# Performance work log

Measured on AMD Instinct MI355X. Metric: run time of the kernel, lower is better.

Reference implementation:

```python
import jax, jax.numpy as jnp
import numpy as np
import math

B, C, T = 4, 512, 2048
LN_EPS = 1e-5

def setup_inputs() -> dict:
    key = jax.random.key(0)
    ks = jax.random.split(key, 12)
    s = 1.0 / math.sqrt(C)
    inp = {
        'feat': jax.random.normal(ks[0], (B, C, T), dtype=jnp.float32),
        'Wq': jax.random.normal(ks[1], (C, C), dtype=jnp.float32) * s,
        'bq': jax.random.normal(ks[2], (C,), dtype=jnp.float32) * s,
        'Wk': jax.random.normal(ks[3], (C, C), dtype=jnp.float32) * s,
        'bk': jax.random.normal(ks[4], (C,), dtype=jnp.float32) * s,
        'Wv': jax.random.normal(ks[5], (C, C), dtype=jnp.float32) * s,
        'bv': jax.random.normal(ks[6], (C,), dtype=jnp.float32) * s,
        'Ws': jax.random.normal(ks[7], (C, C), dtype=jnp.float32) * s,
        'bs': jax.random.normal(ks[8], (C,), dtype=jnp.float32) * s,
        'Wl': jax.random.normal(ks[9], (C,), dtype=jnp.float32) * s,
        'bl': jax.random.normal(ks[10], (1,), dtype=jnp.float32) * s,
    }
    return inp

def reference(feat, Wq, bq, Wk, bk, Wv, bv, Ws, bs, Wl, bl):
    d = feat.shape[1]
    # 1x1 Conv1d == per-position linear over channels. feat: [B,C,T]
    value = jnp.einsum('oc,bct->bto', Wv, feat) + bv          # [B,T,C]
    query = jnp.einsum('oc,bct->bto', Wq, feat) + bq          # [B,T,C]
    key_  = jnp.einsum('oc,bct->bct', Wk, feat) + bk[:, None] # [B,C,T]
    f = jnp.einsum('btc,bcs->bts', query, key_) / math.sqrt(d)
    f = jax.nn.softmax(f, axis=2)                             # [B,T,T]
    y = jnp.einsum('bts,bsc->btc', f, value)                  # [B,T,C]
    f_score = jax.nn.sigmoid(jnp.einsum('btc,c->bt', y, Wl) + bl[0])
    z = jnp.einsum('bts,bsc->btc', 1.0 - f, value)            # [B,T,C]
    b_score = 1.0 - jax.nn.sigmoid(jnp.einsum('btc,c->bt', z, Wl) + bl[0])
    f_score = (f_score + b_score) / 2.0
    y_ct = jnp.einsum('oc,btc->bot', Ws, y) + bs[:, None]     # smooth conv, [B,C,T]
    out = feat + y_ct
    # LayerNorm over (C, T) jointly, default affine (weight=1, bias=0)
    mu = jnp.mean(out, axis=(1, 2), keepdims=True)
    var = jnp.mean(jnp.square(out - mu), axis=(1, 2), keepdims=True)
    out = (out - mu) * jax.lax.rsqrt(var + LN_EPS)
    return out, f_score
```

## Files before the change

### kernel.cpp

```cpp
#include <hip/hip_runtime.h>
#include <hip/hip_bf16.h>

#define BB 4
#define CC 512
#define TT 2048
static constexpr long CT  = (long)CC * TT;
static constexpr long TC  = (long)TT * CC;
static constexpr long TTT = (long)TT * TT;
static constexpr float SM_SCALE = 0.04419417382415922f;

typedef __bf16 bf16;
typedef __attribute__((ext_vector_type(8))) __bf16 bf16x8;
typedef __attribute__((ext_vector_type(4))) __bf16 bf16x4;
typedef __attribute__((ext_vector_type(4))) float f32x4;

__device__ __forceinline__ void load_lds16(const bf16* g, bf16* l)
{
    __builtin_amdgcn_global_load_lds(
        (const __attribute__((address_space(1))) void*)g,
        (__attribute__((address_space(3))) void*)l, 16, 0, 0);
}

template <int TM, int TN, int WR, int WC, int BK>
struct Core {
    static constexpr int THREADS = WR * WC * 64;
    static constexpr int MI = TM / (WR * 16);
    static constexpr int NI = TN / (WC * 16);
    static constexpr int CPR = BK / 8;
    static constexpr int RSH = (BK == 64) ? 3 : 2;
    static constexpr int CMASK = CPR - 1;
    static constexpr int CHUNKS = (TM + TN) * CPR;
    static constexpr int ACH = TM * CPR;
    static constexpr int CPT = CHUNKS / THREADS;
    static_assert(CPT * THREADS == CHUNKS, "chunk divisibility");

    __device__ static __forceinline__ void run(
        const bf16* __restrict__ Ab, const bf16* __restrict__ Bb,
        int K, int m0, int n0, bf16* As, bf16* Bs, f32x4 (&acc)[MI][NI])
    {
        const int tid  = threadIdx.x;
        const int lane = tid & 63;
        const int wid  = tid >> 6;
        const int wr = (wid / WC) * (MI * 16);
        const int wc = (wid % WC) * (NI * 16);
        const int lm = lane & 15;
        const int lq = lane >> 4;
        for (int k0 = 0; k0 < K; k0 += BK) {
#pragma unroll
            for (int i = 0; i < CPT; ++i) {
                int c = tid + i * THREADS;
                if (c < ACH) {
                    int row = c >> RSH;
                    int gc  = (c & CMASK) ^ (row & CMASK);
                    load_lds16(Ab + (long)(m0 + row) * K + k0 + gc * 8, As + c * 8);
                } else {
                    int d = c - ACH;
                    int row = d >> RSH;
                    int gc  = (d & CMASK) ^ (row & CMASK);
                    load_lds16(Bb + (long)(n0 + row) * K + k0 + gc * 8, Bs + d * 8);
                }
            }
            __syncthreads();
#pragma unroll
            for (int ks = 0; ks < BK / 32; ++ks) {
                bf16x8 af[MI], bfr[NI];
#pragma unroll
                for (int i = 0; i < MI; ++i) {
                    int ar = wr + i * 16 + lm;
                    int cc = (ks * 4 + lq) ^ (ar & CMASK);
                    af[i] = *(const bf16x8*)(As + ar * BK + cc * 8);
                }
#pragma unroll
                for (int i = 0; i < NI; ++i) {
                    int br = wc + i * 16 + lm;
                    int cc = (ks * 4 + lq) ^ (br & CMASK);
                    bfr[i] = *(const bf16x8*)(Bs + br * BK + cc * 8);
                }
#pragma unroll
                for (int mi = 0; mi < MI; ++mi)
#pragma unroll
                    for (int ni = 0; ni < NI; ++ni)
                        acc[mi][ni] = __builtin_amdgcn_mfma_f32_16x16x32_bf16(
                            af[mi], bfr[ni], acc[mi][ni], 0, 0, 0);
            }
            __syncthreads();
        }
    }
};

using CO = Core<128, 128, 4, 2, 64>;

struct CoreQV {
    static constexpr int THREADS = 512;
    static constexpr int MI = 2;
    static constexpr int NI = 4;
    static constexpr int BK = 64;
    static constexpr int CPR = 8, RSH = 3, CMASK = 7;
    static constexpr int ACH = 128 * 8;
    static constexpr int CHUNKS = 256 * 8;
    static constexpr int CPT = CHUNKS / THREADS;

    __device__ static __forceinline__ void run(
        const bf16* __restrict__ Ab, const bf16* __restrict__ Bq,
        const bf16* __restrict__ Bv,
        int m0, bf16* As, bf16* Bs, f32x4 (&acc)[MI][NI])
    {
        const int tid  = threadIdx.x;
        const int lane = tid & 63;
        const int wid  = tid >> 6;
        const int wr = (wid / 2) * 32;
        const int wc = (wid % 2) * 64;
        const int lm = lane & 15;
        const int lq = lane >> 4;
        for (int k0 = 0; k0 < 512; k0 += BK) {
#pragma unroll
            for (int i = 0; i < CPT; ++i) {
                int c = tid + i * THREADS;
                if (c < ACH) {
                    int row = c >> RSH;
                    int gc  = (c & CMASK) ^ (row & CMASK);
                    load_lds16(Ab + (long)(m0 + row) * 512 + k0 + gc * 8, As + c * 8);
                } else {
                    int d = c - ACH;
                    int row = d >> RSH;
                    int gc  = (d & CMASK) ^ (row & CMASK);
                    const bf16* src = (row < 64)
                        ? Bq + (long)row * 512
                        : Bv + (long)(row - 64) * 512;
                    load_lds16(src + k0 + gc * 8, Bs + d * 8);
                }
            }
            __syncthreads();
#pragma unroll
            for (int ks = 0; ks < 2; ++ks) {
                bf16x8 af[MI], bfr[NI];
#pragma unroll
                for (int i = 0; i < MI; ++i) {
                    int ar = wr + i * 16 + lm;
                    int cc = (ks * 4 + lq) ^ (ar & CMASK);
                    af[i] = *(const bf16x8*)(As + ar * BK + cc * 8);
                }
#pragma unroll
                for (int i = 0; i < NI; ++i) {
                    int br = wc + i * 16 + lm;
                    int cc = (ks * 4 + lq) ^ (br & CMASK);
                    bfr[i] = *(const bf16x8*)(Bs + br * BK + cc * 8);
                }
#pragma unroll
                for (int mi = 0; mi < MI; ++mi)
#pragma unroll
                    for (int ni = 0; ni < NI; ++ni)
                        acc[mi][ni] = __builtin_amdgcn_mfma_f32_16x16x32_bf16(
                            af[mi], bfr[ni], acc[mi][ni], 0, 0, 0);
            }
            __syncthreads();
        }
    }
};

__global__ __launch_bounds__(512)
void gemm_qv_kernel(const bf16* __restrict__ featT, const bf16* __restrict__ Wq_bf,
                    const bf16* __restrict__ Wv_bf, bf16* __restrict__ Qb,
                    bf16* __restrict__ Vn, const float* __restrict__ bq,
                    const float* __restrict__ bv, const float* __restrict__ wkc,
                    const float* __restrict__ bk, float* __restrict__ qb,
                    const float* __restrict__ Wl, float* __restrict__ vl)
{
    __shared__ bf16 As[128 * 64];
    __shared__ bf16 Bs[128 * 64];
    const int rb = blockIdx.z;
    const int m0 = blockIdx.y * 128;
    const int ng = blockIdx.x;
    const long wofs = (long)(ng * 64) * 512;
    f32x4 acc[2][4] = {};
    CoreQV::run(featT + (long)rb * TC, Wq_bf + wofs, Wv_bf + wofs, m0, As, Bs, acc);

    const int lane = threadIdx.x & 63, wid = threadIdx.x >> 6;
    const int wr = (wid / 2) * 32;
    const bool isV = wid & 1;
    const int lm = lane & 15, lq = lane >> 4;

    if (isV) {
        bf16* outV = Vn + (long)rb * TC;
        float* vlb = vl + (long)rb * TT;
        float vs_[2][4] = {};
#pragma unroll
        for (int mi = 0; mi < 2; ++mi)
#pragma unroll
            for (int ni = 0; ni < 4; ++ni) {
                int n = ng * 64 + ni * 16 + lm;
                float bn = bv[n], wn = Wl[n];
#pragma unroll
                for (int r = 0; r < 4; ++r) {
                    int m = m0 + wr + mi * 16 + lq * 4 + r;
                    float v = acc[mi][ni][r] + bn;
                    outV[(long)m * 512 + n] = (bf16)v;
                    vs_[mi][r] += v * wn;
                }
            }
#pragma unroll
        for (int mi = 0; mi < 2; ++mi)
#pragma unroll
            for (int r = 0; r < 4; ++r) {
                float s = vs_[mi][r];
                s += __shfl_xor(s, 1, 64); s += __shfl_xor(s, 2, 64);
                s += __shfl_xor(s, 4, 64); s += __shfl_xor(s, 8, 64);
                if (lm == 0)
                    atomicAdd(vlb + m0 + wr + mi * 16 + lq * 4 + r, s);
            }
    } else {
        bf16* out = Qb + (long)rb * TC;
        float* qbb = qb + (long)rb * TT;
        float rs[2][4] = {};
#pragma unroll
        for (int mi = 0; mi < 2; ++mi)
#pragma unroll
            for (int ni = 0; ni < 4; ++ni) {
                int n = ng * 64 + ni * 16 + lm;
                float bn = bq[n], wn = wkc[n], kn = bk[n];
#pragma unroll
                for (int r = 0; r < 4; ++r) {
                    int m = m0 + wr + mi * 16 + lq * 4 + r;
                    float v = acc[mi][ni][r] + bn;
                    rs[mi][r] += v * kn;
                    out[(long)m * 512 + n] = (bf16)(v * wn);
                }
            }
#pragma unroll
        for (int mi = 0; mi < 2; ++mi)
#pragma unroll
            for (int r = 0; r < 4; ++r) {
                float s = rs[mi][r];
                s += __shfl_xor(s, 1, 64); s += __shfl_xor(s, 2, 64);
                s += __shfl_xor(s, 4, 64); s += __shfl_xor(s, 8, 64);
                if (lm == 0)
                    atomicAdd(qbb + m0 + wr + mi * 16 + lq * 4 + r, s);
            }
    }
}

__global__ __launch_bounds__(512, 2)
void gemm_s256_kernel(const bf16* __restrict__ Qb, const bf16* __restrict__ featT,
                      bf16* __restrict__ S, const float* __restrict__ qb,
                      float* __restrict__ rsum, const float* __restrict__ vl,
                      float* __restrict__ u)
{
    __shared__ __align__(16) bf16 lds[2][2][256 * 64];
    const int id   = blockIdx.x;
    const int xcd  = id & 7, sIdx = id >> 3;
    const int bz   = xcd >> 1;
    const int n0   = (sIdx & 7) * 256;
    const int m0   = (((xcd & 1) << 2) + (sIdx >> 3)) * 256;
    const bf16* __restrict__ Ab = Qb + (long)bz * TC;
    const bf16* __restrict__ Bb = featT + (long)bz * TC;

    const int tid  = threadIdx.x;
    const int lane = tid & 63;
    const int wid  = tid >> 6;
    const int lm = lane & 15, lq = lane >> 4;
    const int wrb = (wid >> 2) * 64;
    const int wcb = (wid & 3) * 32;

    f32x4 acc[8][4] = {};

#define FENCE asm volatile("" ::: "memory")

#define STAGE_HT(t, op, h)                                                    \
    do {                                                                      \
        const bf16* gp_ = (op) ? Bb : Ab;                                     \
        const int  br_  = ((op) ? n0 : m0) + (h) * 128;                       \
        bf16* lp_ = &lds[(t) & 1][op][(h) * 128 * 64];                        \
        _Pragma("unroll")                                                     \
        for (int i_ = 0; i_ < 2; ++i_) {                                      \
            int c_ = tid + i_ * 512;                                          \
            int r_ = c_ >> 3;                                                 \
            int g_ = (c_ & 7) ^ (r_ & 7);                                     \
            load_lds16(gp_ + (long)(br_ + r_) * 512 + (t) * 64 + g_ * 8,      \
                       lp_ + c_ * 8);                                         \
        }                                                                     \
    } while (0)

#define PHASE(t, qm, qn, doSt, st, sop, sh, doVm)                             \
    do {                                                                      \
        bf16x8 af[2][4], bfr[2][2];                                           \
        const bf16* Al_ = lds[(t) & 1][0];                                    \
        const bf16* Bl_ = lds[(t) & 1][1];                                    \
        _Pragma("unroll")                                                     \
        for (int ks = 0; ks < 2; ++ks) {                                      \
            _Pragma("unroll")                                                 \
            for (int j = 0; j < 4; ++j) {                                     \
                int ar = (qm) * 128 + wrb + j * 16 + lm;                      \
                int cc = (ks * 4 + lq) ^ (ar & 7);                            \
                af[ks][j] = *(const bf16x8*)(Al_ + ar * 64 + cc * 8);         \
            }                                                                 \
            _Pragma("unroll")                                                 \
            for (int j = 0; j < 2; ++j) {                                     \
                int br = (qn) * 128 + wcb + j * 16 + lm;                      \
                int cc = (ks * 4 + lq) ^ (br & 7);                            \
                bfr[ks][j] = *(const bf16x8*)(Bl_ + br * 64 + cc * 8);        \
            }                                                                 \
        }                                                                     \
        if (doSt) STAGE_HT(st, sop, sh);                                      \
        if (doVm) {                                                           \
            if ((t) < 6) asm volatile("s_waitcnt vmcnt(4)" ::: "memory");     \
            else         asm volatile("s_waitcnt vmcnt(0)" ::: "memory");     \
        }                                                                     \
        FENCE; __builtin_amdgcn_s_barrier(); FENCE;                           \
        __builtin_amdgcn_s_setprio(1);                                        \
        _Pragma("unroll")                                                     \
        for (int ks = 0; ks < 2; ++ks)                                        \
            _Pragma("unroll")                                                 \
            for (int j = 0; j < 4; ++j)                                       \
                _Pragma("unroll")                                             \
                for (int j2 = 0; j2 < 2; ++j2)                                \
                    acc[(qm) * 4 + j][(qn) * 2 + j2] =                        \
                        __builtin_amdgcn_mfma_f32_16x16x32_bf16(              \
                            af[ks][j], bfr[ks][j2],                           \
                            acc[(qm) * 4 + j][(qn) * 2 + j2], 0, 0, 0);       \
        __builtin_amdgcn_s_setprio(0);                                        \
        FENCE; __builtin_amdgcn_s_barrier(); FENCE;                           \
    } while (0)

    STAGE_HT(0, 0, 0); STAGE_HT(0, 1, 0); STAGE_HT(0, 0, 1); STAGE_HT(0, 1, 1);
    STAGE_HT(1, 0, 0); STAGE_HT(1, 1, 0);
    asm volatile("s_waitcnt vmcnt(4)" ::: "memory");
    FENCE; __builtin_amdgcn_s_barrier(); FENCE;

    for (int t = 0; t < 8; ++t) {
        PHASE(t, 0, 0, t + 1 < 8, t + 1, 0, 1, false);
        PHASE(t, 0, 1, t + 1 < 8, t + 1, 1, 1, false);
        PHASE(t, 1, 0, t + 2 < 8, t + 2, 0, 0, false);
        PHASE(t, 1, 1, t + 2 < 8, t + 2, 1, 0, true);
    }
#undef PHASE
#undef STAGE_HT
#undef FENCE

    bf16* outp = S + (long)bz * TTT;
    const float* qbb = qb + (long)bz * TT;
    const float* vlb = vl + (long)bz * TT;
    float* rsb = rsum + (long)bz * TT;
    float* ub  = u + (long)bz * TT;
#pragma unroll
    for (int mi = 0; mi < 8; ++mi) {
        const int mrow = m0 + (mi >> 2) * 128 + wrb + (mi & 3) * 16 + lq * 4;
        const f32x4 qv = *(const f32x4*)(qbb + mrow);
        float rp[4] = {0.f, 0.f, 0.f, 0.f};
        float up[4] = {0.f, 0.f, 0.f, 0.f};
#pragma unroll
        for (int ni = 0; ni < 4; ++ni) {
            const int ncol = n0 + (ni >> 1) * 128 + wcb + (ni & 1) * 16 + lm;
            const float vlv = vlb[ncol];
#pragma unroll
            for (int r = 0; r < 4; ++r) {
                float p = __expf((acc[mi][ni][r] + qv[r]) * SM_SCALE);
                outp[(long)(mrow + r) * 2048 + ncol] = (bf16)p;
                rp[r] += p;
                up[r] += p * vlv;
            }
        }
#pragma unroll
        for (int r = 0; r < 4; ++r) {
            float s2 = rp[r], s3 = up[r];
            s2 += __shfl_xor(s2, 1, 64); s2 += __shfl_xor(s2, 2, 64);
            s2 += __shfl_xor(s2, 4, 64); s2 += __shfl_xor(s2, 8, 64);
            s3 += __shfl_xor(s3, 1, 64); s3 += __shfl_xor(s3, 2, 64);
            s3 += __shfl_xor(s3, 4, 64); s3 += __shfl_xor(s3, 8, 64);
            if (lm == 0) {
                atomicAdd(rsb + mrow + r, s2);
                atomicAdd(ub + mrow + r, s3);
            }
        }
    }
}

__global__ __launch_bounds__(512)
void gemm_vs_kernel(const bf16* __restrict__ Vn, const bf16* __restrict__ Ws_bf,
                    bf16* __restrict__ Vpt)
{
    __shared__ bf16 As[128 * 64];
    __shared__ bf16 Bs[128 * 64];
    const int id = blockIdx.x;
    const int xcd = id & 7, s = id >> 3;
    const int bz = xcd >> 1;
    const int m0 = (((xcd & 1) << 1) + (s >> 4)) * 128;
    const int n0 = (s & 15) * 128;
    f32x4 acc[2][4] = {};
    CO::run(Ws_bf, Vn + (long)bz * TC, 512, m0, n0, As, Bs, acc);

    const int lane = threadIdx.x & 63, wid = threadIdx.x >> 6;
    const int wr = (wid / 2) * 32, wc = (wid % 2) * 64;
    const int lm = lane & 15, lq = lane >> 4;
    bf16* out = Vpt + (long)bz * CT;
#pragma unroll
    for (int mi = 0; mi < 2; ++mi)
#pragma unroll
        for (int ni = 0; ni < 4; ++ni) {
            int n = n0 + wc + ni * 16 + lm;
#pragma unroll
            for (int r = 0; r < 4; ++r) {
                int m = m0 + wr + mi * 16 + lq * 4 + r;
                out[(long)m * 2048 + n] = (bf16)acc[mi][ni][r];
            }
        }
}

__global__ __launch_bounds__(512)
void gemm_out_kernel(const bf16* __restrict__ S, const bf16* __restrict__ Vpt,
                     float* __restrict__ out, const float* __restrict__ bs,
                     const float* __restrict__ feat,
                     const float* __restrict__ rsum, double* __restrict__ stats)
{
    __shared__ bf16 As[128 * 64];
    __shared__ bf16 Bs[128 * 64];
    __shared__ float red[16];
    const int id = blockIdx.x;
    const int xcd = id & 7, s = id >> 3;
    const int bz = xcd >> 1;
    const int n0 = (s & 3) * 128;
    const int m0 = (((xcd & 1) << 3) + (s >> 2)) * 128;
    f32x4 acc[2][4] = {};
    CO::run(S + (long)bz * TTT, Vpt + (long)bz * CT, 2048, m0, n0, As, Bs, acc);

    const int tid = threadIdx.x;
    const int lane = tid & 63, wid = tid >> 6;
    const int wr = (wid / 2) * 32, wc = (wid % 2) * 64;
    const int lm = lane & 15, lq = lane >> 4;
    const float* rsb = rsum + (long)bz * TT;
    float inv[2][4];
#pragma unroll
    for (int mi = 0; mi < 2; ++mi) {
        int mrow = m0 + wr + mi * 16 + lq * 4;
        f32x4 rv = *(const f32x4*)(rsb + mrow);
#pragma unroll
        for (int r = 0; r < 4; ++r) inv[mi][r] = 1.f / rv[r];
    }
    float s1 = 0.f, s2 = 0.f;
#pragma unroll
    for (int mi = 0; mi < 2; ++mi)
#pragma unroll
        for (int ni = 0; ni < 4; ++ni) {
            int mrow = m0 + wr + mi * 16 + lq * 4;
            int n = n0 + wc + ni * 16 + lm;
            long off = (long)bz * CT + (long)n * TT + mrow;
            f32x4 fv = *(const f32x4*)(feat + off);
            float bn = bs[n];
            f32x4 res;
#pragma unroll
            for (int r = 0; r < 4; ++r) {
                float v = acc[mi][ni][r] * inv[mi][r] + bn + fv[r];
                res[r] = v;
                s1 += v;
                s2 += v * v;
            }
            *(f32x4*)(out + off) = res;
        }
#pragma unroll
    for (int off = 32; off; off >>= 1) {
        s1 += __shfl_xor(s1, off, 64);
        s2 += __shfl_xor(s2, off, 64);
    }
    if (lane == 0) { red[wid] = s1; red[8 + wid] = s2; }
    __syncthreads();
    if (tid == 0) {
        double t1 = 0.0, t2 = 0.0;
#pragma unroll
        for (int w = 0; w < 8; ++w) { t1 += red[w]; t2 += red[8 + w]; }
        atomicAdd(stats + bz * 2, t1);
        atomicAdd(stats + bz * 2 + 1, t2);
    }
}

__global__ __launch_bounds__(256)
void prep_kernel(const float* __restrict__ feat, bf16* __restrict__ featT,
                 const float* __restrict__ Wq, const float* __restrict__ Wv,
                 const float* __restrict__ Ws, bf16* __restrict__ Wbf,
                 const float* __restrict__ Wk, const float* __restrict__ Wl,
                 const float* __restrict__ bv, float* __restrict__ wkc,
                 float* __restrict__ wvl, float* __restrict__ wlbv,
                 float* __restrict__ frp, float* __restrict__ qb,
                 float* __restrict__ u, float* __restrict__ rsum,
                 double* __restrict__ stats, float* __restrict__ vl)
{
    const int blk = blockIdx.x;
    const int tid = threadIdx.x;
    if (blk < 4096) {
        __shared__ float tile[32][33];
        __shared__ float sfr[4][32];
        const int b  = blk >> 10;
        const int c0 = ((blk & 1023) >> 6) * 32;
        const int tt = blk & 63;
        const int t0 = tt * 32;
        const int tx = tid & 31;
        const int ty = tid >> 5;
#pragma unroll
        for (int j = 0; j < 4; ++j) {
            int c = c0 + ty + j * 8;
            tile[ty + j * 8][tx] = feat[(long)b * CT + (long)c * TT + t0 + tx];
        }
        __syncthreads();
        float ps = 0.f;
#pragma unroll
        for (int j = 0; j < 4; ++j) {
            int tl = ty + j * 8;
            int t = t0 + tl;
            int c = c0 + tx;
            float v = tile[tx][tl];
            ps += v;
            featT[(long)b * TC + (long)t * CC + c] = (bf16)v;
        }
        const int wid = tid >> 6;
        ps += __shfl_xor(ps, 32, 64);
        if ((tid & 63) < 32) sfr[wid][tx] = ps;
        __syncthreads();
        if (tid < 32) {
            float s = sfr[0][tid] + sfr[1][tid] + sfr[2][tid] + sfr[3][tid];
            frp[(((long)b * 64 + tt) << 9) + c0 + tid] = s;
        }
    } else if (blk < 4480) {
        long gid = (long)(blk - 4096) * 256 + tid;
        long idx = gid * 8;
        int w = (int)(idx >> 18);
        long off = idx & 262143;
        const float* src = (w == 0) ? Wq : (w == 1) ? Wv : Ws;
        f32x4 a = *(const f32x4*)(src + off);
        f32x4 b = *(const f32x4*)(src + off + 4);
        bf16x8 o;
#pragma unroll
        for (int j = 0; j < 4; ++j) { o[j] = (bf16)a[j]; o[4 + j] = (bf16)b[j]; }
        *(bf16x8*)(Wbf + idx) = o;
    } else {
        int mid = (blk - 4480) * 256 + tid;
        if (mid < 512) {
            float s = 0.f;
            for (int o = 0; o < 512; ++o) s += Wk[o * 512 + mid];
            wkc[mid] = s;
        } else if (mid < 1024) {
            int k = mid - 512;
            float s = 0.f;
            for (int c = 0; c < 512; ++c) s += Wl[c] * Wv[c * 512 + k];
            wvl[k] = s;
        } else if (mid < 1088) {
            int lane = mid - 1024;
            float s = 0.f;
#pragma unroll
            for (int j = 0; j < 8; ++j) s += Wl[lane + 64 * j] * bv[lane + 64 * j];
#pragma unroll
            for (int off = 32; off; off >>= 1) s += __shfl_xor(s, off, 64);
            if (lane == 0) wlbv[0] = s;
        } else if (mid >= 1152 && mid < 1160) {
            stats[mid - 1152] = 0.0;
        } else if (mid >= 4096 && mid < 12288) {
            qb[mid - 4096] = 0.f;
        } else if (mid >= 12288 && mid < 20480) {
            u[mid - 12288] = 0.f;
        } else if (mid >= 20480 && mid < 28672) {
            rsum[mid - 20480] = 0.f;
        } else if (mid >= 28672 && mid < 36864) {
            vl[mid - 28672] = 0.f;
        }
    }
}

__global__ __launch_bounds__(256)
void ln_score_kernel(float* __restrict__ out, const double* __restrict__ stats,
                     const float* __restrict__ u, const float* __restrict__ frp,
                     const float* __restrict__ wvl, const float* __restrict__ wlbv,
                     const float* __restrict__ blp, const float* __restrict__ rsum)
{
    if (blockIdx.x < 4096) {
        long i = ((long)blockIdx.x * 256 + threadIdx.x) * 4;
        int b = (int)(i >> 20);
        const double n = 1048576.0;
        double mu  = stats[b * 2] / n;
        double var = stats[b * 2 + 1] / n - mu * mu;
        float rs = (float)(1.0 / sqrt(var + 1e-5));
        float muf = (float)mu;
        f32x4 v = *(f32x4*)(out + i);
#pragma unroll
        for (int j = 0; j < 4; ++j) v[j] = (v[j] - muf) * rs;
        *(f32x4*)(out + i) = v;
    } else {
        const int b = blockIdx.x - 4096;
        __shared__ float ssv[4];
        const int tid = threadIdx.x, lane = tid & 63, wid = tid >> 6;
        const float* fb = frp + ((long)b * 64 << 9);
        float s0 = 0.f, s1 = 0.f;
#pragma unroll 8
        for (int k = 0; k < 64; ++k) {
            s0 += fb[(k << 9) + tid];
            s1 += fb[(k << 9) + tid + 256];
        }
        float p = s0 * wvl[tid] + s1 * wvl[tid + 256];
#pragma unroll
        for (int off = 32; off; off >>= 1) p += __shfl_xor(p, off, 64);
        if (lane == 0) ssv[wid] = p;
        __syncthreads();
        const float sv = ssv[0] + ssv[1] + ssv[2] + ssv[3] + 2048.f * wlbv[0];
        const float bl0 = blp[0];
#pragma unroll
        for (int j = 0; j < 8; ++j) {
            int t = tid + j * 256;
            float uu = u[(long)b * TT + t] / rsum[(long)b * TT + t];
            float uf = uu + bl0;
            float vf = sv - uu + bl0;
            float fs  = 1.f / (1.f + __expf(-uf));
            float bsc = 1.f - 1.f / (1.f + __expf(-vf));
            out[(long)BB * CT + (long)b * TT + t] = 0.5f * (fs + bsc);
        }
    }
}

extern "C" void kernel_launch(void* const* d_in, const int* in_sizes, int n_in,
                              void* d_out, int out_size, void* d_ws, size_t ws_size,
                              hipStream_t stream)
{
    const float* feat = (const float*)d_in[0];
    const float* Wq   = (const float*)d_in[1];
    const float* bq   = (const float*)d_in[2];
    const float* Wk   = (const float*)d_in[3];
    const float* bk   = (const float*)d_in[4];
    const float* Wv   = (const float*)d_in[5];
    const float* bv   = (const float*)d_in[6];
    const float* Ws   = (const float*)d_in[7];
    const float* bs   = (const float*)d_in[8];
    const float* Wl   = (const float*)d_in[9];
    const float* bl   = (const float*)d_in[10];
    float* out = (float*)d_out;

    if (ws_size < 69316736) return;
    char* ws = (char*)d_ws;
    bf16* featT  = (bf16*)(ws);
    bf16* Wbf    = (bf16*)(ws + 8388608);
    bf16* Qb     = (bf16*)(ws + 9961472);
    bf16* Vn     = (bf16*)(ws + 18350080);
    bf16* Vpt    = (bf16*)(ws + 26738688);
    float* vl    = (float*)(ws + 26738688);
    bf16* S      = (bf16*)(ws + 35127296);
    float* wkc   = (float*)(ws + 68689920);
    float* wvl   = (float*)(ws + 68691968);
    float* wlbv  = (float*)(ws + 68694016);
    float* qb    = (float*)(ws + 68694080);
    double* stats= (double*)(ws + 68726848);
    float* u     = (float*)(ws + 68726912);
    float* rsum  = (float*)(ws + 68759680);
    float* frp   = (float*)(ws + 68792448);

    bf16* Wq_bf = Wbf;
    bf16* Wv_bf = Wbf + 262144;
    bf16* Ws_bf = Wbf + 524288;

    prep_kernel<<<4624, 256, 0, stream>>>(feat, featT, Wq, Wv, Ws, Wbf, Wk, Wl, bv,
                                          wkc, wvl, wlbv, frp, qb, u, rsum, stats, vl);
    gemm_qv_kernel<<<dim3(8, 16, 4), 512, 0, stream>>>(
        featT, Wq_bf, Wv_bf, Qb, Vn, bq, bv, wkc, bk, qb, Wl, vl);
    gemm_s256_kernel<<<256, 512, 0, stream>>>(Qb, featT, S, qb, rsum, vl, u);
    gemm_vs_kernel<<<256, 512, 0, stream>>>(Vn, Ws_bf, Vpt);
    gemm_out_kernel<<<256, 512, 0, stream>>>(S, Vpt, out, bs, feat, rsum, stats);
    ln_score_kernel<<<4100, 256, 0, stream>>>(out, stats, u, frp, wvl, wlbv, bl, rsum);
}
```

Measured before the change: 222.1 us.

## Double-buffer LDS tiles in QV, VS and output GEMMs with async prefetch

The generic GEMM core and the QV core are replaced with two-stage pipelined versions. Tile t+2 is loaded with global_load_lds into the alternate LDS buffer while MFMAs run on the current tile, using explicit vmcnt waits and raw s_barrier instead of __syncthreads. Fragments are read into registers before the barrier so the buffer can be refilled early, and MFMA priority is raised with s_setprio. This doubles LDS use per block to 64KB and adds register pressure, which may lower occupancy.

```diff
diff --git a/kernel.cpp b/kernel.cpp
--- a/kernel.cpp
+++ b/kernel.cpp
@@ -21,8 +21,10 @@
         (__attribute__((address_space(3))) void*)l, 16, 0, 0);
 }
 
+#define FENCE asm volatile("" ::: "memory")
+
 template <int TM, int TN, int WR, int WC, int BK>
-struct Core {
+struct CorePipe {
     static constexpr int THREADS = WR * WC * 64;
     static constexpr int MI = TM / (WR * 16);
     static constexpr int NI = TN / (WC * 16);
@@ -33,6 +35,29 @@
     static constexpr int ACH = TM * CPR;
     static constexpr int CPT = CHUNKS / THREADS;
     static_assert(CPT * THREADS == CHUNKS, "chunk divisibility");
+    static_assert(CPT == 4, "vmcnt literals below assume 4 loads/thread/tile");
+
+    __device__ static __forceinline__ void stage(
+        const bf16* __restrict__ Ab, const bf16* __restrict__ Bb,
+        int K, int m0, int n0, int t, int p, bf16* As, bf16* Bs, int tid)
+    {
+#pragma unroll
+        for (int i = 0; i < CPT; ++i) {
+            int c = tid + i * THREADS;
+            if (c < ACH) {
+                int row = c >> RSH;
+                int gc  = (c & CMASK) ^ (row & CMASK);
+                load_lds16(Ab + (long)(m0 + row) * K + t * BK + gc * 8,
+                           As + p * (TM * BK) + c * 8);
+            } else {
+                int d = c - ACH;
+                int row = d >> RSH;
+                int gc  = (d & CMASK) ^ (row & CMASK);
+                load_lds16(Bb + (long)(n0 + row) * K + t * BK + gc * 8,
+                           Bs + p * (TN * BK) + d * 8);
+            }
+        }
+    }
 
     __device__ static __forceinline__ void run(
         const bf16* __restrict__ Ab, const bf16* __restrict__ Bb,
@@ -45,52 +70,62 @@
         const int wc = (wid % WC) * (NI * 16);
         const int lm = lane & 15;
         const int lq = lane >> 4;
-        for (int k0 = 0; k0 < K; k0 += BK) {
-#pragma unroll
-            for (int i = 0; i < CPT; ++i) {
-                int c = tid + i * THREADS;
-                if (c < ACH) {
-                    int row = c >> RSH;
-                    int gc  = (c & CMASK) ^ (row & CMASK);
-                    load_lds16(Ab + (long)(m0 + row) * K + k0 + gc * 8, As + c * 8);
-                } else {
-                    int d = c - ACH;
-                    int row = d >> RSH;
-                    int gc  = (d & CMASK) ^ (row & CMASK);
-                    load_lds16(Bb + (long)(n0 + row) * K + k0 + gc * 8, Bs + d * 8);
-                }
-            }
-            __syncthreads();
+        const int nt = K / BK;
+
+        stage(Ab, Bb, K, m0, n0, 0, 0, As, Bs, tid);
+        stage(Ab, Bb, K, m0, n0, 1, 1, As, Bs, tid);
+        asm volatile("s_waitcnt vmcnt(4)" ::: "memory");
+        FENCE; __builtin_amdgcn_s_barrier(); FENCE;
+
+        for (int t = 0; t < nt; ++t) {
+            const int p = t & 1;
+            const bf16* Ap = As + p * (TM * BK);
+            const bf16* Bp = Bs + p * (TN * BK);
+            bf16x8 af[BK / 32][MI], bfr[BK / 32][NI];
 #pragma unroll
             for (int ks = 0; ks < BK / 32; ++ks) {
-                bf16x8 af[MI], bfr[NI];
 #pragma unroll
                 for (int i = 0; i < MI; ++i) {
                     int ar = wr + i * 16 + lm;
                     int cc = (ks * 4 + lq) ^ (ar & CMASK);
-                    af[i] = *(const bf16x8*)(As + ar * BK + cc * 8);
+                    af[ks][i] = *(const bf16x8*)(Ap + ar * BK + cc * 8);
                 }
 #pragma unroll
                 for (int i = 0; i < NI; ++i) {
                     int br = wc + i * 16 + lm;
                     int cc = (ks * 4 + lq) ^ (br & CMASK);
-                    bfr[i] = *(const bf16x8*)(Bs + br * BK + cc * 8);
+                    bfr[ks][i] = *(const bf16x8*)(Bp + br * BK + cc * 8);
                 }
+            }
+            asm volatile("s_waitcnt lgkmcnt(0)" ::: "memory");
+            __builtin_amdgcn_sched_barrier(0);
+            FENCE; __builtin_amdgcn_s_barrier(); FENCE;
+            if (t + 2 < nt)
+                stage(Ab, Bb, K, m0, n0, t + 2, p, As, Bs, tid);
+            __builtin_amdgcn_s_setprio(1);
+#pragma unroll
+            for (int ks = 0; ks < BK / 32; ++ks)
 #pragma unroll
                 for (int mi = 0; mi < MI; ++mi)
 #pragma unroll
                     for (int ni = 0; ni < NI; ++ni)
                         acc[mi][ni] = __builtin_amdgcn_mfma_f32_16x16x32_bf16(
-                            af[mi], bfr[ni], acc[mi][ni], 0, 0, 0);
-            }
-            __syncthreads();
+                            af[ks][mi], bfr[ks][ni], acc[mi][ni], 0, 0, 0);
+            __builtin_amdgcn_s_setprio(0);
+            if (t + 1 < nt) {
+                if (t + 2 < nt)
+                    asm volatile("s_waitcnt vmcnt(4)" ::: "memory");
+                else
+                    asm volatile("s_waitcnt vmcnt(0)" ::: "memory");
+                FENCE; __builtin_amdgcn_s_barrier(); FENCE;
+            }
         }
     }
 };
 
-using CO = Core<128, 128, 4, 2, 64>;
-
-struct CoreQV {
+using CP = CorePipe<128, 128, 4, 2, 64>;
+
+struct CoreQVPipe {
     static constexpr int THREADS = 512;
     static constexpr int MI = 2;
     static constexpr int NI = 4;
@@ -99,6 +134,31 @@
     static constexpr int ACH = 128 * 8;
     static constexpr int CHUNKS = 256 * 8;
     static constexpr int CPT = CHUNKS / THREADS;
+
+    __device__ static __forceinline__ void stage(
+        const bf16* __restrict__ Ab, const bf16* __restrict__ Bq,
+        const bf16* __restrict__ Bv, int m0, int t, int p,
+        bf16* As, bf16* Bs, int tid)
+    {
+#pragma unroll
+        for (int i = 0; i < CPT; ++i) {
+            int c = tid + i * THREADS;
+            if (c < ACH) {
+                int row = c >> RSH;
+                int gc  = (c & CMASK) ^ (row & CMASK);
+                load_lds16(Ab + (long)(m0 + row) * 512 + t * 64 + gc * 8,
+                           As + p * (128 * 64) + c * 8);
+            } else {
+                int d = c - ACH;
+                int row = d >> RSH;
+                int gc  = (d & CMASK) ^ (row & CMASK);
+                const bf16* src = (row < 64)
+                    ? Bq + (long)row * 512
+                    : Bv + (long)(row - 64) * 512;
+                load_lds16(src + t * 64 + gc * 8, Bs + p * (128 * 64) + d * 8);
+            }
+        }
+    }
 
     __device__ static __forceinline__ void run(
         const bf16* __restrict__ Ab, const bf16* __restrict__ Bq,
@@ -112,48 +172,55 @@
         const int wc = (wid % 2) * 64;
         const int lm = lane & 15;
         const int lq = lane >> 4;
-        for (int k0 = 0; k0 < 512; k0 += BK) {
-#pragma unroll
-            for (int i = 0; i < CPT; ++i) {
-                int c = tid + i * THREADS;
-                if (c < ACH) {
-                    int row = c >> RSH;
-                    int gc  = (c & CMASK) ^ (row & CMASK);
-                    load_lds16(Ab + (long)(m0 + row) * 512 + k0 + gc * 8, As + c * 8);
-                } else {
-                    int d = c - ACH;
-                    int row = d >> RSH;
-                    int gc  = (d & CMASK) ^ (row & CMASK);
-                    const bf16* src = (row < 64)
-                        ? Bq + (long)row * 512
-                        : Bv + (long)(row - 64) * 512;
-                    load_lds16(src + k0 + gc * 8, Bs + d * 8);
-                }
-            }
-            __syncthreads();
+        const int nt = 8;
+
+        stage(Ab, Bq, Bv, m0, 0, 0, As, Bs, tid);
+        stage(Ab, Bq, Bv, m0, 1, 1, As, Bs, tid);
+        asm volatile("s_waitcnt vmcnt(4)" ::: "memory");
+        FENCE; __builtin_amdgcn_s_barrier(); FENCE;
+
+        for (int t = 0; t < nt; ++t) {
+            const int p = t & 1;
+            const bf16* Ap = As + p * (128 * 64);
+            const bf16* Bp = Bs + p * (128 * 64);
+            bf16x8 af[2][MI], bfr[2][NI];
 #pragma unroll
             for (int ks = 0; ks < 2; ++ks) {
-                bf16x8 af[MI], bfr[NI];
 #pragma unroll
                 for (int i = 0; i < MI; ++i) {
                     int ar = wr + i * 16 + lm;
                     int cc = (ks * 4 + lq) ^ (ar & CMASK);
-                    af[i] = *(const bf16x8*)(As + ar * BK + cc * 8);
+                    af[ks][i] = *(const bf16x8*)(Ap + ar * BK + cc * 8);
                 }
 #pragma unroll
                 for (int i = 0; i < NI; ++i) {
                     int br = wc + i * 16 + lm;
                     int cc = (ks * 4 + lq) ^ (br & CMASK);
-                    bfr[i] = *(const bf16x8*)(Bs + br * BK + cc * 8);
+                    bfr[ks][i] = *(const bf16x8*)(Bp + br * BK + cc * 8);
                 }
+            }
+            asm volatile("s_waitcnt lgkmcnt(0)" ::: "memory");
+            __builtin_amdgcn_sched_barrier(0);
+            FENCE; __builtin_amdgcn_s_barrier(); FENCE;
+            if (t + 2 < nt)
+                stage(Ab, Bq, Bv, m0, t + 2, p, As, Bs, tid);
+            __builtin_amdgcn_s_setprio(1);
+#pragma unroll
+            for (int ks = 0; ks < 2; ++ks)
 #pragma unroll
                 for (int mi = 0; mi < MI; ++mi)
 #pragma unroll
                     for (int ni = 0; ni < NI; ++ni)
                         acc[mi][ni] = __builtin_amdgcn_mfma_f32_16x16x32_bf16(
-                            af[mi], bfr[ni], acc[mi][ni], 0, 0, 0);
-            }
-            __syncthreads();
+                            af[ks][mi], bfr[ks][ni], acc[mi][ni], 0, 0, 0);
+            __builtin_amdgcn_s_setprio(0);
+            if (t + 1 < nt) {
+                if (t + 2 < nt)
+                    asm volatile("s_waitcnt vmcnt(4)" ::: "memory");
+                else
+                    asm volatile("s_waitcnt vmcnt(0)" ::: "memory");
+                FENCE; __builtin_amdgcn_s_barrier(); FENCE;
+            }
         }
     }
 };
@@ -166,14 +233,14 @@
                     const float* __restrict__ bk, float* __restrict__ qb,
                     const float* __restrict__ Wl, float* __restrict__ vl)
 {
-    __shared__ bf16 As[128 * 64];
-    __shared__ bf16 Bs[128 * 64];
+    __shared__ __align__(16) bf16 As[2 * 128 * 64];
+    __shared__ __align__(16) bf16 Bs[2 * 128 * 64];
     const int rb = blockIdx.z;
     const int m0 = blockIdx.y * 128;
     const int ng = blockIdx.x;
     const long wofs = (long)(ng * 64) * 512;
     f32x4 acc[2][4] = {};
-    CoreQV::run(featT + (long)rb * TC, Wq_bf + wofs, Wv_bf + wofs, m0, As, Bs, acc);
+    CoreQVPipe::run(featT + (long)rb * TC, Wq_bf + wofs, Wv_bf + wofs, m0, As, Bs, acc);
 
     const int lane = threadIdx.x & 63, wid = threadIdx.x >> 6;
     const int wr = (wid / 2) * 32;
@@ -262,8 +329,6 @@
     const int wcb = (wid & 3) * 32;
 
     f32x4 acc[8][4] = {};
-
-#define FENCE asm volatile("" ::: "memory")
 
 #define STAGE_HT(t, op, h)                                                    \
     do {                                                                      \
@@ -334,7 +399,6 @@
     }
 #undef PHASE
 #undef STAGE_HT
-#undef FENCE
 
     bf16* outp = S + (long)bz * TTT;
     const float* qbb = qb + (long)bz * TT;
@@ -378,15 +442,15 @@
 void gemm_vs_kernel(const bf16* __restrict__ Vn, const bf16* __restrict__ Ws_bf,
                     bf16* __restrict__ Vpt)
 {
-    __shared__ bf16 As[128 * 64];
-    __shared__ bf16 Bs[128 * 64];
+    __shared__ __align__(16) bf16 As[2 * 128 * 64];
+    __shared__ __align__(16) bf16 Bs[2 * 128 * 64];
     const int id = blockIdx.x;
     const int xcd = id & 7, s = id >> 3;
     const int bz = xcd >> 1;
     const int m0 = (((xcd & 1) << 1) + (s >> 4)) * 128;
     const int n0 = (s & 15) * 128;
     f32x4 acc[2][4] = {};
-    CO::run(Ws_bf, Vn + (long)bz * TC, 512, m0, n0, As, Bs, acc);
+    CP::run(Ws_bf, Vn + (long)bz * TC, 512, m0, n0, As, Bs, acc);
 
     const int lane = threadIdx.x & 63, wid = threadIdx.x >> 6;
     const int wr = (wid / 2) * 32, wc = (wid % 2) * 64;
@@ -411,8 +475,8 @@
                      const float* __restrict__ feat,
                      const float* __restrict__ rsum, double* __restrict__ stats)
 {
-    __shared__ bf16 As[128 * 64];
-    __shared__ bf16 Bs[128 * 64];
+    __shared__ __align__(16) bf16 As[2 * 128 * 64];
+    __shared__ __align__(16) bf16 Bs[2 * 128 * 64];
     __shared__ float red[16];
     const int id = blockIdx.x;
     const int xcd = id & 7, s = id >> 3;
@@ -420,7 +484,7 @@
     const int n0 = (s & 3) * 128;
     const int m0 = (((xcd & 1) << 3) + (s >> 2)) * 128;
     f32x4 acc[2][4] = {};
-    CO::run(S + (long)bz * TTT, Vpt + (long)bz * CT, 2048, m0, n0, As, Bs, acc);
+    CP::run(S + (long)bz * TTT, Vpt + (long)bz * CT, 2048, m0, n0, As, Bs, acc);
 
     const int tid = threadIdx.x;
     const int lane = tid & 63, wid = tid >> 6;
```

New measurement: 211.7 us. 4.7% less time.
